# Performance work log

Hardware: AMD Instinct MI355X
Metric: run time of the kernel (lower is better)

The kernel has to match this reference:

```python
import jax, jax.numpy as jnp
import numpy as np

IN_CH = 256
OUT_CH = 256
K = 3
STRIDE = 1
PAD = 1
NUM_EMB = 8


def setup_inputs() -> dict:
    key = jax.random.key(0)
    ks = jax.random.split(key, 6)
    B, H, W = 16, 64, 64
    x = jax.random.normal(ks[0], (B, IN_CH, H, W), dtype=jnp.float32)
    kernal_embed = jax.random.normal(ks[1], (NUM_EMB, IN_CH, OUT_CH, K, K), dtype=jnp.float32)
    # 1x1 conv params (stored as a dense [out,in] matrix) + bias
    cls_conv_w = jax.random.normal(ks[2], (IN_CH, IN_CH), dtype=jnp.float32) / np.sqrt(IN_CH)
    cls_conv_b = jax.random.normal(ks[3], (IN_CH,), dtype=jnp.float32) * 0.01
    cls_dense_w = jax.random.normal(ks[4], (NUM_EMB, IN_CH), dtype=jnp.float32) / np.sqrt(IN_CH)
    cls_dense_b = jax.random.normal(ks[5], (NUM_EMB,), dtype=jnp.float32) * 0.01
    return {"x": x, "kernal_embed": kernal_embed, "cls_conv_w": cls_conv_w,
            "cls_conv_b": cls_conv_b, "cls_dense_w": cls_dense_w, "cls_dense_b": cls_dense_b}


def reference(x, kernal_embed, cls_conv_w, cls_conv_b, cls_dense_w, cls_dense_b):
    B, C, H, W = x.shape
    # 1x1 conv -> global avg pool -> dense -> softmax weights over embeddings
    w = jnp.einsum('bchw,dc->bdhw', x, cls_conv_w) + cls_conv_b[None, :, None, None]
    pooled = jnp.mean(w, axis=(2, 3))                       # (B, C)
    logits = pooled @ cls_dense_w.T + cls_dense_b           # (B, E)
    mix = jax.nn.softmax(logits, axis=1)                    # (B, E)
    # Per-sample kernel synthesis: (B, in, out, k, k)
    kern = jnp.einsum('be,eiojk->biojk', mix, kernal_embed)
    # Faithful to torch .view(-1, in, k, k): raw reshape (mixes in/out axes as in original)
    kern = kern.reshape(B, OUT_CH, IN_CH, K, K)
    # Grouped conv with groups=B == per-sample conv via vmap
    def conv1(xi, wi):
        # xi: (C, H, W), wi: (out, in, k, k)
        return jax.lax.conv_general_dilated(
            xi[None], wi, window_strides=(STRIDE, STRIDE),
            padding=[(PAD, PAD), (PAD, PAD)],
            dimension_numbers=('NCHW', 'OIHW', 'NCHW'))[0]
    out = jax.vmap(conv1)(x, kern)                          # (B, out, H, W)
    return out
```

## Files before the change

kernel.cpp:

```cpp
#include <hip/hip_runtime.h>
#include <stdint.h>

#define B_  16
#define C_  256
#define H_  64
#define W_  64
#define P_  4096
#define E_  8
#define HP_ 66

typedef __bf16 bf16x8 __attribute__((ext_vector_type(8)));
typedef float  f32x4  __attribute__((ext_vector_type(4)));

__device__ __forceinline__ unsigned short f2bf(float f) {
    union { float f; unsigned int u; } v; v.f = f;
    unsigned int u = v.u;
    unsigned int r = (u + 0x7fffu + ((u >> 16) & 1u)) >> 16;
    return (unsigned short)r;
}

__device__ __forceinline__ void async_load16(const void* g, void* l) {
    __builtin_amdgcn_global_load_lds(
        (const __attribute__((address_space(1))) void*)g,
        (__attribute__((address_space(3))) void*)l, 16, 0, 0);
}

__global__ void k_xpose(const float* __restrict__ x, unsigned short* __restrict__ Xp,
                        float* __restrict__ xsum) {
    const int bid0 = blockIdx.x;
    const int tid = threadIdx.x;
    if (bid0 >= B_ * H_ * 4) {
        const int gid = (bid0 - B_ * H_ * 4) * 256 + tid;
        const int pix = gid >> 5;
        const int chunk = gid & 31;
        const int b = pix / 260;
        const int j = pix - b * 260;
        int h, w;
        if (j < 66)       { h = 0;  w = j; }
        else if (j < 132) { h = 65; w = j - 66; }
        else { int jj = j - 132; h = 1 + (jj & 63); w = (jj < 64) ? 0 : 65; }
        const uint4 z = {0u, 0u, 0u, 0u};
        *(uint4*)(Xp + ((size_t)((b * HP_ + h) * HP_ + w) << 8) + chunk * 8) = z;
        return;
    }
    const int b  = bid0 >> 8;
    const int h  = (bid0 >> 2) & 63;
    const int cg = bid0 & 3;
    const int c0 = cg << 6;
    __shared__ float tile[64][65];
    {
        const int ci = tid >> 2, wseg = tid & 3;
        const float* src = x + ((size_t)(b * 256 + c0 + ci) << 12) + (h << 6) + wseg * 16;
        float s = 0.f;
#pragma unroll
        for (int i = 0; i < 4; ++i) {
            float4 v = *(const float4*)(src + i * 4);
            tile[ci][wseg * 16 + i * 4 + 0] = v.x;
            tile[ci][wseg * 16 + i * 4 + 1] = v.y;
            tile[ci][wseg * 16 + i * 4 + 2] = v.z;
            tile[ci][wseg * 16 + i * 4 + 3] = v.w;
            s += v.x + v.y + v.z + v.w;
        }
        s += __shfl_down(s, 1, 64);
        s += __shfl_down(s, 2, 64);
        if ((tid & 3) == 0) atomicAdd(&xsum[b * 256 + c0 + ci], s);
    }
    __syncthreads();
    {
        const int w = tid >> 2, cs = tid & 3;
        unsigned short ov[16] __attribute__((aligned(16)));
#pragma unroll
        for (int k = 0; k < 16; ++k) ov[k] = f2bf(tile[cs * 16 + k][w]);
        unsigned short* dst = Xp + ((size_t)((b * HP_ + h + 1) * HP_ + (w + 1)) << 8) + c0 + cs * 16;
        ((uint4*)dst)[0] = ((const uint4*)ov)[0];
        ((uint4*)dst)[1] = ((const uint4*)ov)[1];
    }
}

__global__ void k_mix(const float* __restrict__ xsum,
                      const float* __restrict__ cw, const float* __restrict__ cb,
                      const float* __restrict__ dw, const float* __restrict__ db,
                      float* __restrict__ mix) {
    const int b = blockIdx.x, tid = threadIdx.x;
    const int wave = tid >> 6, lane = tid & 63;
    __shared__ __align__(16) float sxm[256];
    __shared__ __align__(16) float spool[256];
    __shared__ float sl[8];
    sxm[tid] = xsum[b * 256 + tid] * (1.0f / P_);
    __syncthreads();
    const float4 xm4 = *(const float4*)(sxm + lane * 4);
#pragma unroll 4
    for (int i = 0; i < 64; ++i) {
        const int d = i * 4 + wave;
        const float4 w4 = *(const float4*)(cw + (size_t)d * 256 + lane * 4);
        float p = w4.x * xm4.x + w4.y * xm4.y + w4.z * xm4.z + w4.w * xm4.w;
        for (int off = 32; off; off >>= 1) p += __shfl_down(p, off, 64);
        if (lane == 0) spool[d] = p + cb[d];
    }
    __syncthreads();
    const float4 pp4 = *(const float4*)(spool + lane * 4);
#pragma unroll
    for (int i = 0; i < 2; ++i) {
        const int e = i * 4 + wave;
        const float4 w4 = *(const float4*)(dw + (size_t)e * 256 + lane * 4);
        float p = w4.x * pp4.x + w4.y * pp4.y + w4.z * pp4.z + w4.w * pp4.w;
        for (int off = 32; off; off >>= 1) p += __shfl_down(p, off, 64);
        if (lane == 0) sl[e] = p + db[e];
    }
    __syncthreads();
    if (tid < 8) {
        float m = sl[0];
        for (int e = 1; e < 8; ++e) m = fmaxf(m, sl[e]);
        float den = 0.f;
        for (int e = 0; e < 8; ++e) den += __expf(sl[e] - m);
        mix[b * 8 + tid] = __expf(sl[tid] - m) / den;
    }
}

__global__ void k_mixkern(const float* __restrict__ KE, const float* __restrict__ mix,
                          unsigned short* __restrict__ Wg) {
    const int o    = blockIdx.x >> 1;
    const int half = blockIdx.x & 1;
    const int ic0  = half << 7;
    const int tid  = threadIdx.x;
    __shared__ __align__(16) float s[8][1152];
    __shared__ float smix[128];
    if (tid < 128) smix[tid] = mix[tid];
#pragma unroll
    for (int e = 0; e < 8; ++e) {
        const float4* src4 = (const float4*)(KE + (size_t)(e * 256 + o) * 2304 + ic0 * 9);
        float4* d4 = (float4*)&s[e][0];
        d4[tid] = src4[tid];
        if (tid < 32) d4[256 + tid] = src4[256 + tid];
    }
    __syncthreads();
    const int icl = tid & 127;
    const int b0  = (tid >> 7) << 3;
#pragma unroll
    for (int t = 0; t < 9; ++t) {
        float v[8];
#pragma unroll
        for (int e = 0; e < 8; ++e) v[e] = s[e][icl * 9 + t];
#pragma unroll
        for (int bb = 0; bb < 8; ++bb) {
            const int b = b0 + bb;
            float acc = 0.f;
#pragma unroll
            for (int e = 0; e < 8; ++e) acc += smix[b * 8 + e] * v[e];
            Wg[((size_t)(b * 256 + o) * 9 + t) * 256 + ic0 + icl] = f2bf(acc);
        }
    }
}

__global__ __launch_bounds__(256) void k_gemm(const unsigned short* __restrict__ Wg,
                                              const unsigned short* __restrict__ Xp,
                                              float* __restrict__ out) {
    __shared__ __align__(16) unsigned short lA[128 * 64];
    __shared__ __align__(16) unsigned short lB[128 * 64];
    const int tid = threadIdx.x;
    const int bid = blockIdx.x;
    const int xcd = bid & 7;
    const int g   = bid >> 3;
    const int b   = xcd + ((g >> 6) << 3);
    const int rem = g & 63;
    const int ot  = rem & 1;
    const int rp  = rem >> 1;
    const int o0  = ot << 7;
    const int h0  = rp << 1;

    const int wid  = tid >> 6;
    const int lane = tid & 63;
    const int wm   = wid >> 1;
    const int wn   = wid & 1;
    const int ql   = lane & 15;
    const int quad = lane >> 4;
    const int sw   = ql & 7;

    const int srow = tid >> 3;
    const int sseg = tid & 7;
    const int csrc = sseg ^ (srow & 7);

    f32x4 acc[4][4];
#pragma unroll
    for (int i = 0; i < 4; ++i)
#pragma unroll
        for (int j = 0; j < 4; ++j) acc[i][j] = (f32x4)0.0f;

    char* lAb = (char*)lA;
    char* lBb = (char*)lB;
    const size_t abase = (size_t)(b * 256 + o0 + srow) * 9 * 256 + csrc * 8;

    for (int t = 0; t < 9; ++t) {
        const int kh = t / 3;
        const int kw = t - kh * 3;
        for (int kc = 0; kc < 4; ++kc) {
#pragma unroll
            for (int j = 0; j < 4; ++j) {
                const unsigned short* ga = Wg + abase + (size_t)j * 32 * 9 * 256
                                           + (size_t)t * 256 + kc * 64;
                async_load16(ga, lAb + tid * 16 + j * 4096);
            }
#pragma unroll
            for (int j = 0; j < 4; ++j) {
                const int pix = srow + 32 * j;
                const int pr  = pix >> 6;
                const int w   = pix & 63;
                const unsigned short* gb = Xp
                    + ((size_t)((b * HP_ + h0 + pr + kh) * HP_ + (w + kw)) << 8)
                    + kc * 64 + csrc * 8;
                async_load16(gb, lBb + tid * 16 + j * 4096);
            }
            __syncthreads();
#pragma unroll
            for (int kk = 0; kk < 2; ++kk) {
                bf16x8 af[4], bv[4];
#pragma unroll
                for (int mi = 0; mi < 4; ++mi)
                    af[mi] = *(const bf16x8*)(lAb + (wm * 64 + mi * 16 + ql) * 128
                                              + ((((kk << 2) | quad) ^ sw) << 4));
#pragma unroll
                for (int ni = 0; ni < 4; ++ni)
                    bv[ni] = *(const bf16x8*)(lBb + (wn * 64 + ni * 16 + ql) * 128
                                              + ((((kk << 2) | quad) ^ sw) << 4));
#pragma unroll
                for (int mi = 0; mi < 4; ++mi)
#pragma unroll
                    for (int ni = 0; ni < 4; ++ni)
                        acc[mi][ni] = __builtin_amdgcn_mfma_f32_16x16x32_bf16(
                            af[mi], bv[ni], acc[mi][ni], 0, 0, 0);
            }
            __syncthreads();
        }
    }

    const int h = h0 + wn;
#pragma unroll
    for (int mi = 0; mi < 4; ++mi) {
        const int o = o0 + wm * 64 + mi * 16 + quad * 4;
#pragma unroll
        for (int ni = 0; ni < 4; ++ni) {
            const int w = ni * 16 + ql;
            float* po = out + ((size_t)(b * 256 + o) << 12) + (h << 6) + w;
#pragma unroll
            for (int r = 0; r < 4; ++r) po[(size_t)r << 12] = acc[mi][ni][r];
        }
    }
}

extern "C" void kernel_launch(void* const* d_in, const int* in_sizes, int n_in,
                              void* d_out, int out_size, void* d_ws, size_t ws_size,
                              hipStream_t stream) {
    const float* x  = (const float*)d_in[0];
    const float* KE = (const float*)d_in[1];
    const float* cw = (const float*)d_in[2];
    const float* cb = (const float*)d_in[3];
    const float* dw = (const float*)d_in[4];
    const float* db = (const float*)d_in[5];
    float* out = (float*)d_out;

    char* ws = (char*)d_ws;
    float* xsum           = (float*)(ws + 0);
    float* mix            = (float*)(ws + 16384);
    unsigned short* Wg    = (unsigned short*)(ws + 32768);
    unsigned short* Xp    = (unsigned short*)(ws + 32768 + 18874368);

    hipMemsetAsync(xsum, 0, B_ * C_ * sizeof(float), stream);
    k_xpose  <<<dim3(B_ * H_ * 4 + 520), dim3(256), 0, stream>>>(x, Xp, xsum);
    k_mix    <<<dim3(B_),                dim3(256), 0, stream>>>(xsum, cw, cb, dw, db, mix);
    k_mixkern<<<dim3(C_ * 2),            dim3(256), 0, stream>>>(KE, mix, Wg);
    k_gemm   <<<dim3(B_ * 2 * 32),       dim3(256), 0, stream>>>(Wg, Xp, out);
}
```

Measured before the change: 291.7 us.

## Switch conv GEMM to 32x32x16 MFMA and replace pooling atomics with partial sums

The GEMM inner loop now uses 32x32x16 bf16 MFMA tiles (2x2 per wave) instead of 16x16x32 tiles (4x4 per wave). This halves the number of LDS fragment reads per wave and uses the larger matrix instruction, at the cost of a reworked output index mapping. Separately, the channel sums for pooling are written as per-row partials and reduced in k_mix, which removes the atomics and the memset. The xpart buffer aliases the Wg region. That is safe only because k_mix consumes xpart before k_mixkern writes Wg on the same stream.

```diff
diff --git a/kernel.cpp b/kernel.cpp
--- a/kernel.cpp
+++ b/kernel.cpp
@@ -11,6 +11,7 @@
 
 typedef __bf16 bf16x8 __attribute__((ext_vector_type(8)));
 typedef float  f32x4  __attribute__((ext_vector_type(4)));
+typedef float  f32x16 __attribute__((ext_vector_type(16)));
 
 __device__ __forceinline__ unsigned short f2bf(float f) {
     union { float f; unsigned int u; } v; v.f = f;
@@ -26,7 +27,7 @@
 }
 
 __global__ void k_xpose(const float* __restrict__ x, unsigned short* __restrict__ Xp,
-                        float* __restrict__ xsum) {
+                        float* __restrict__ xpart) {
     const int bid0 = blockIdx.x;
     const int tid = threadIdx.x;
     if (bid0 >= B_ * H_ * 4) {
@@ -63,7 +64,7 @@
         }
         s += __shfl_down(s, 1, 64);
         s += __shfl_down(s, 2, 64);
-        if ((tid & 3) == 0) atomicAdd(&xsum[b * 256 + c0 + ci], s);
+        if ((tid & 3) == 0) xpart[((size_t)(b * 64 + h) << 8) + c0 + ci] = s;
     }
     __syncthreads();
     {
@@ -77,7 +78,7 @@
     }
 }
 
-__global__ void k_mix(const float* __restrict__ xsum,
+__global__ void k_mix(const float* __restrict__ xpart,
                       const float* __restrict__ cw, const float* __restrict__ cb,
                       const float* __restrict__ dw, const float* __restrict__ db,
                       float* __restrict__ mix) {
@@ -86,7 +87,13 @@
     __shared__ __align__(16) float sxm[256];
     __shared__ __align__(16) float spool[256];
     __shared__ float sl[8];
-    sxm[tid] = xsum[b * 256 + tid] * (1.0f / P_);
+    {
+        const float* xp = xpart + ((size_t)b << 14) + tid;
+        float s = 0.f;
+#pragma unroll
+        for (int h = 0; h < 64; ++h) s += xp[h << 8];
+        sxm[tid] = s * (1.0f / P_);
+    }
     __syncthreads();
     const float4 xm4 = *(const float4*)(sxm + lane * 4);
 #pragma unroll 4
@@ -172,19 +179,19 @@
     const int lane = tid & 63;
     const int wm   = wid >> 1;
     const int wn   = wid & 1;
-    const int ql   = lane & 15;
-    const int quad = lane >> 4;
-    const int sw   = ql & 7;
+    const int r5   = lane & 31;
+    const int half = lane >> 5;
+    const int sw   = lane & 7;
 
     const int srow = tid >> 3;
     const int sseg = tid & 7;
     const int csrc = sseg ^ (srow & 7);
 
-    f32x4 acc[4][4];
-#pragma unroll
-    for (int i = 0; i < 4; ++i)
-#pragma unroll
-        for (int j = 0; j < 4; ++j) acc[i][j] = (f32x4)0.0f;
+    f32x16 acc[2][2];
+#pragma unroll
+    for (int i = 0; i < 2; ++i)
+#pragma unroll
+        for (int j = 0; j < 2; ++j) acc[i][j] = (f32x16)0.0f;
 
     char* lAb = (char*)lA;
     char* lBb = (char*)lB;
@@ -212,37 +219,38 @@
             }
             __syncthreads();
 #pragma unroll
-            for (int kk = 0; kk < 2; ++kk) {
-                bf16x8 af[4], bv[4];
-#pragma unroll
-                for (int mi = 0; mi < 4; ++mi)
-                    af[mi] = *(const bf16x8*)(lAb + (wm * 64 + mi * 16 + ql) * 128
-                                              + ((((kk << 2) | quad) ^ sw) << 4));
-#pragma unroll
-                for (int ni = 0; ni < 4; ++ni)
-                    bv[ni] = *(const bf16x8*)(lBb + (wn * 64 + ni * 16 + ql) * 128
-                                              + ((((kk << 2) | quad) ^ sw) << 4));
-#pragma unroll
-                for (int mi = 0; mi < 4; ++mi)
-#pragma unroll
-                    for (int ni = 0; ni < 4; ++ni)
-                        acc[mi][ni] = __builtin_amdgcn_mfma_f32_16x16x32_bf16(
+            for (int s = 0; s < 4; ++s) {
+                const int ch = ((2 * s + half) ^ sw) << 4;
+                bf16x8 af[2], bv[2];
+#pragma unroll
+                for (int mi = 0; mi < 2; ++mi)
+                    af[mi] = *(const bf16x8*)(lAb + (wm * 64 + mi * 32 + r5) * 128 + ch);
+#pragma unroll
+                for (int ni = 0; ni < 2; ++ni)
+                    bv[ni] = *(const bf16x8*)(lBb + (wn * 64 + ni * 32 + r5) * 128 + ch);
+#pragma unroll
+                for (int mi = 0; mi < 2; ++mi)
+#pragma unroll
+                    for (int ni = 0; ni < 2; ++ni)
+                        acc[mi][ni] = __builtin_amdgcn_mfma_f32_32x32x16_bf16(
                             af[mi], bv[ni], acc[mi][ni], 0, 0, 0);
             }
             __syncthreads();
         }
     }
 
-    const int h = h0 + wn;
-#pragma unroll
-    for (int mi = 0; mi < 4; ++mi) {
-        const int o = o0 + wm * 64 + mi * 16 + quad * 4;
-#pragma unroll
-        for (int ni = 0; ni < 4; ++ni) {
-            const int w = ni * 16 + ql;
-            float* po = out + ((size_t)(b * 256 + o) << 12) + (h << 6) + w;
-#pragma unroll
-            for (int r = 0; r < 4; ++r) po[(size_t)r << 12] = acc[mi][ni][r];
+#pragma unroll
+    for (int mi = 0; mi < 2; ++mi) {
+        const int ob = o0 + wm * 64 + mi * 32 + half * 4;
+#pragma unroll
+        for (int ni = 0; ni < 2; ++ni) {
+            const int p = wn * 64 + ni * 32 + r5;
+            const int h = h0 + (p >> 6);
+            const int w = p & 63;
+            float* po = out + ((size_t)(b * 256 + ob) << 12) + (h << 6) + w;
+#pragma unroll
+            for (int r = 0; r < 16; ++r)
+                po[(size_t)((r & 3) + 8 * (r >> 2)) << 12] = acc[mi][ni][r];
         }
     }
 }
@@ -259,14 +267,13 @@
     float* out = (float*)d_out;
 
     char* ws = (char*)d_ws;
-    float* xsum           = (float*)(ws + 0);
-    float* mix            = (float*)(ws + 16384);
+    float* mix            = (float*)(ws + 0);
+    float* xpart          = (float*)(ws + 32768);
     unsigned short* Wg    = (unsigned short*)(ws + 32768);
     unsigned short* Xp    = (unsigned short*)(ws + 32768 + 18874368);
 
-    hipMemsetAsync(xsum, 0, B_ * C_ * sizeof(float), stream);
-    k_xpose  <<<dim3(B_ * H_ * 4 + 520), dim3(256), 0, stream>>>(x, Xp, xsum);
-    k_mix    <<<dim3(B_),                dim3(256), 0, stream>>>(xsum, cw, cb, dw, db, mix);
+    k_xpose  <<<dim3(B_ * H_ * 4 + 520), dim3(256), 0, stream>>>(x, Xp, xpart);
+    k_mix    <<<dim3(B_),                dim3(256), 0, stream>>>(xpart, cw, cb, dw, db, mix);
     k_mixkern<<<dim3(C_ * 2),            dim3(256), 0, stream>>>(KE, mix, Wg);
     k_gemm   <<<dim3(B_ * 2 * 32),       dim3(256), 0, stream>>>(Wg, Xp, out);
 }
```

New measurement: 304.5 us. 1.04x slower.

## Double-buffer GEMM B tiles, load A directly to registers, drop atomics

Applied to the files above, without the earlier changes.

The conv GEMM now keeps the weight operand A in registers, loaded straight from global memory, instead of staging it through LDS. The pixel operand B is double-buffered in LDS so the next K-chunk loads while the current one feeds MFMAs. Separately, the channel-sum atomics and their memset are replaced by per-row partial sums that k_mix reduces. The partial-sum buffer aliases the Wg workspace region; this is safe only because k_mix consumes it before k_mixkern overwrites Wg. The unstaged A loads may also be less coalesced than the old LDS path.

```diff
diff --git a/kernel.cpp b/kernel.cpp
--- a/kernel.cpp
+++ b/kernel.cpp
@@ -26,7 +26,7 @@
 }
 
 __global__ void k_xpose(const float* __restrict__ x, unsigned short* __restrict__ Xp,
-                        float* __restrict__ xsum) {
+                        float* __restrict__ xpart) {
     const int bid0 = blockIdx.x;
     const int tid = threadIdx.x;
     if (bid0 >= B_ * H_ * 4) {
@@ -63,7 +63,7 @@
         }
         s += __shfl_down(s, 1, 64);
         s += __shfl_down(s, 2, 64);
-        if ((tid & 3) == 0) atomicAdd(&xsum[b * 256 + c0 + ci], s);
+        if ((tid & 3) == 0) xpart[((size_t)(b * 64 + h) << 8) + c0 + ci] = s;
     }
     __syncthreads();
     {
@@ -77,7 +77,7 @@
     }
 }
 
-__global__ void k_mix(const float* __restrict__ xsum,
+__global__ void k_mix(const float* __restrict__ xpart,
                       const float* __restrict__ cw, const float* __restrict__ cb,
                       const float* __restrict__ dw, const float* __restrict__ db,
                       float* __restrict__ mix) {
@@ -86,7 +86,13 @@
     __shared__ __align__(16) float sxm[256];
     __shared__ __align__(16) float spool[256];
     __shared__ float sl[8];
-    sxm[tid] = xsum[b * 256 + tid] * (1.0f / P_);
+    {
+        const float* xp = xpart + ((size_t)b << 14) + tid;
+        float s = 0.f;
+#pragma unroll
+        for (int h = 0; h < 64; ++h) s += xp[h << 8];
+        sxm[tid] = s * (1.0f / P_);
+    }
     __syncthreads();
     const float4 xm4 = *(const float4*)(sxm + lane * 4);
 #pragma unroll 4
@@ -155,8 +161,7 @@
 __global__ __launch_bounds__(256) void k_gemm(const unsigned short* __restrict__ Wg,
                                               const unsigned short* __restrict__ Xp,
                                               float* __restrict__ out) {
-    __shared__ __align__(16) unsigned short lA[128 * 64];
-    __shared__ __align__(16) unsigned short lB[128 * 64];
+    __shared__ __align__(16) unsigned short lB[2][128 * 64];
     const int tid = threadIdx.x;
     const int bid = blockIdx.x;
     const int xcd = bid & 7;
@@ -186,52 +191,79 @@
 #pragma unroll
         for (int j = 0; j < 4; ++j) acc[i][j] = (f32x4)0.0f;
 
-    char* lAb = (char*)lA;
-    char* lBb = (char*)lB;
-    const size_t abase = (size_t)(b * 256 + o0 + srow) * 9 * 256 + csrc * 8;
-
-    for (int t = 0; t < 9; ++t) {
-        const int kh = t / 3;
-        const int kw = t - kh * 3;
-        for (int kc = 0; kc < 4; ++kc) {
-#pragma unroll
-            for (int j = 0; j < 4; ++j) {
-                const unsigned short* ga = Wg + abase + (size_t)j * 32 * 9 * 256
-                                           + (size_t)t * 256 + kc * 64;
-                async_load16(ga, lAb + tid * 16 + j * 4096);
-            }
-#pragma unroll
-            for (int j = 0; j < 4; ++j) {
-                const int pix = srow + 32 * j;
-                const int pr  = pix >> 6;
-                const int w   = pix & 63;
-                const unsigned short* gb = Xp
-                    + ((size_t)((b * HP_ + h0 + pr + kh) * HP_ + (w + kw)) << 8)
-                    + kc * 64 + csrc * 8;
-                async_load16(gb, lBb + tid * 16 + j * 4096);
-            }
-            __syncthreads();
-#pragma unroll
-            for (int kk = 0; kk < 2; ++kk) {
-                bf16x8 af[4], bv[4];
-#pragma unroll
-                for (int mi = 0; mi < 4; ++mi)
-                    af[mi] = *(const bf16x8*)(lAb + (wm * 64 + mi * 16 + ql) * 128
-                                              + ((((kk << 2) | quad) ^ sw) << 4));
-#pragma unroll
-                for (int ni = 0; ni < 4; ++ni)
-                    bv[ni] = *(const bf16x8*)(lBb + (wn * 64 + ni * 16 + ql) * 128
-                                              + ((((kk << 2) | quad) ^ sw) << 4));
-#pragma unroll
-                for (int mi = 0; mi < 4; ++mi)
-#pragma unroll
-                    for (int ni = 0; ni < 4; ++ni)
-                        acc[mi][ni] = __builtin_amdgcn_mfma_f32_16x16x32_bf16(
-                            af[mi], bv[ni], acc[mi][ni], 0, 0, 0);
-            }
-            __syncthreads();
+    const unsigned short* apm[4];
+#pragma unroll
+    for (int mi = 0; mi < 4; ++mi)
+        apm[mi] = Wg + (size_t)(b * 256 + o0 + wm * 64 + mi * 16 + ql) * 2304 + quad * 8;
+
+    const unsigned short* bpj[4];
+#pragma unroll
+    for (int j = 0; j < 4; ++j) {
+        const int pix = srow + 32 * j;
+        const int pr  = pix >> 6;
+        const int w   = pix & 63;
+        bpj[j] = Xp + ((size_t)((b * HP_ + h0 + pr) * HP_ + w) << 8) + csrc * 8;
+    }
+
+#define STAGE_B(I, BUF) do {                                                  \
+    const int t_  = (I) >> 2;                                                 \
+    const int kh_ = (t_ * 11) >> 5;                                           \
+    const int kw_ = t_ - kh_ * 3;                                             \
+    const size_t soff_ = ((size_t)(kh_ * HP_ + kw_) << 8) + (((I) & 3) << 6); \
+    char* lbb_ = (char*)lB[BUF];                                              \
+    _Pragma("unroll")                                                         \
+    for (int j = 0; j < 4; ++j)                                               \
+        async_load16(bpj[j] + soff_, lbb_ + tid * 16 + j * 4096);             \
+} while (0)
+
+#define LOAD_A(I, DST) do {                                                   \
+    const size_t aoff_ = (size_t)(I) * 64;                                    \
+    _Pragma("unroll")                                                         \
+    for (int mi = 0; mi < 4; ++mi) {                                          \
+        (DST)[mi][0] = *(const bf16x8*)(apm[mi] + aoff_);                     \
+        (DST)[mi][1] = *(const bf16x8*)(apm[mi] + aoff_ + 32);                \
+    }                                                                         \
+} while (0)
+
+#define MFMA_PHASE(AF, BUF) do {                                              \
+    const char* lbb_ = (const char*)lB[BUF];                                  \
+    _Pragma("unroll")                                                         \
+    for (int kk = 0; kk < 2; ++kk) {                                          \
+        bf16x8 bv[4];                                                         \
+        _Pragma("unroll")                                                     \
+        for (int ni = 0; ni < 4; ++ni)                                        \
+            bv[ni] = *(const bf16x8*)(lbb_ + (wn * 64 + ni * 16 + ql) * 128   \
+                                      + ((((kk << 2) | quad) ^ sw) << 4));    \
+        _Pragma("unroll")                                                     \
+        for (int mi = 0; mi < 4; ++mi)                                        \
+            _Pragma("unroll")                                                 \
+            for (int ni = 0; ni < 4; ++ni)                                    \
+                acc[mi][ni] = __builtin_amdgcn_mfma_f32_16x16x32_bf16(        \
+                    (AF)[mi][kk], bv[ni], acc[mi][ni], 0, 0, 0);              \
+    }                                                                         \
+} while (0)
+
+    bf16x8 aA[4][2], aB_[4][2];
+    STAGE_B(0, 0);
+    LOAD_A(0, aA);
+    __syncthreads();
+
+    for (int i = 0; i < 36; i += 2) {
+        STAGE_B(i + 1, 1);
+        LOAD_A(i + 1, aB_);
+        MFMA_PHASE(aA, 0);
+        __syncthreads();
+        if (i + 2 < 36) {
+            STAGE_B(i + 2, 0);
+            LOAD_A(i + 2, aA);
         }
-    }
+        MFMA_PHASE(aB_, 1);
+        __syncthreads();
+    }
+
+#undef STAGE_B
+#undef LOAD_A
+#undef MFMA_PHASE
 
     const int h = h0 + wn;
 #pragma unroll
@@ -259,14 +291,13 @@
     float* out = (float*)d_out;
 
     char* ws = (char*)d_ws;
-    float* xsum           = (float*)(ws + 0);
-    float* mix            = (float*)(ws + 16384);
+    float* mix            = (float*)(ws + 0);
+    float* xpart          = (float*)(ws + 32768);
     unsigned short* Wg    = (unsigned short*)(ws + 32768);
     unsigned short* Xp    = (unsigned short*)(ws + 32768 + 18874368);
 
-    hipMemsetAsync(xsum, 0, B_ * C_ * sizeof(float), stream);
-    k_xpose  <<<dim3(B_ * H_ * 4 + 520), dim3(256), 0, stream>>>(x, Xp, xsum);
-    k_mix    <<<dim3(B_),                dim3(256), 0, stream>>>(xsum, cw, cb, dw, db, mix);
+    k_xpose  <<<dim3(B_ * H_ * 4 + 520), dim3(256), 0, stream>>>(x, Xp, xpart);
+    k_mix    <<<dim3(B_),                dim3(256), 0, stream>>>(xpart, cw, cb, dw, db, mix);
     k_mixkern<<<dim3(C_ * 2),            dim3(256), 0, stream>>>(KE, mix, Wg);
     k_gemm   <<<dim3(B_ * 2 * 32),       dim3(256), 0, stream>>>(Wg, Xp, out);
 }
```

Measured after the change: 384.4 us. 31.8% more time.
